# Performance work log

Measured on AMD Instinct MI355X. Metric: run time of the kernel, lower is better.

## Reference

```python
import jax, jax.numpy as jnp
import numpy as np

N, C, H, W = 2, 8, 256, 512
K = 9   # kernel_size
D = 1   # dilation


def setup_inputs() -> dict:
    key = jax.random.key(0)
    k1, k2, k3 = jax.random.split(key, 3)
    x_in = jax.random.normal(k1, (N, C, H, W), dtype=jnp.float32)
    filters = jax.random.normal(k2, (N, K * K, H, W), dtype=jnp.float32)
    filters_biases = jax.random.normal(k3, (N, 1, H, W), dtype=jnp.float32)
    return {"x_in": x_in, "filters": filters, "filters_biases": filters_biases}


def reference(x_in, filters, filters_biases):
    # Dynamic (per-pixel) filtering: out[n,c,h,w] = sum_{i,j} x_pad[n,c,h+i*d,w+j*d] * filters[n,i*K+j,h,w] + bias
    # Equivalent to torch: unfold -> [N,C,K*K,H,W], multiply by filters [N,1,K*K,H,W], sum over K*K, add bias.
    # Fused accumulation over the K*K taps avoids materializing the K*K-times larger im2col tensor.
    k, d = K, D
    p = d * (k - 1) // 2  # 'same' padding used by im2col_layer
    n, c, h, w = x_in.shape
    xp = jnp.pad(x_in, ((0, 0), (0, 0), (p, p), (p, p)))
    out = jnp.zeros_like(x_in)
    for i in range(k):          # fixed small kernel loop (81 taps), unrolled by jit
        for j in range(k):
            tap = filters[:, None, i * k + j]                  # [N,1,H,W]
            out = out + xp[:, :, i * d:i * d + h, j * d:j * d + w] * tap
    return out + filters_biases
```

## Files before the change

### kernel.cpp

```cpp
#include <hip/hip_runtime.h>

#define CC 8
#define HH 256
#define WW 512
#define KK 9
#define XF 272

__global__ __launch_bounds__(256, 4) void dynfilter_kernel(
    const float* __restrict__ x,
    const float* __restrict__ filt,
    const float* __restrict__ fbias,
    float* __restrict__ out)
{
    __shared__ __align__(16) float xs[4][2][2][XF];

    const int tid  = threadIdx.x;
    const int wv   = tid >> 6;
    const int lane = tid & 63;

    const int bid0 = blockIdx.x;
    const int bid  = ((bid0 & 7) << 7) | (bid0 >> 3);

    const int seg = bid & 1;
    const int h   = (bid >> 1) & 255;
    const int n   = bid >> 9;

    const int w0      = seg * 256 + (lane << 2);
    const int wstage0 = seg * 256 - 4;

    const size_t HW = (size_t)HH * WW;
    const int c0 = wv << 1;

    const float* xr0  = x + (size_t)(n * CC + c0)     * HW + wstage0;
    const float* xr1  = x + (size_t)(n * CC + c0 + 1) * HW + wstage0;
    const float* fptr = filt + ((size_t)(n * 81) * HH + h) * WW + w0;

    float acc0[4], acc1[4];
    {
        const float4 b4 = *(const float4*)(fbias + ((size_t)(n * HH + h)) * WW + w0);
        acc0[0]=b4.x; acc0[1]=b4.y; acc0[2]=b4.z; acc0[3]=b4.w;
        acc1[0]=b4.x; acc1[1]=b4.y; acc1[2]=b4.z; acc1[3]=b4.w;
    }

    const int wlo = wstage0 + (lane << 2);
    const int whi = wstage0 + 256 + (lane << 2);
    const bool lo_ok = (unsigned)wlo < (unsigned)WW;
    const bool hi_ok = (lane < 2) && ((unsigned)whi < (unsigned)WW);

    {
        const int hh = h - 4;
        const bool rowok = hh >= 0;
        const float* s0 = xr0 + (size_t)hh * WW;
        const float* s1 = xr1 + (size_t)hh * WW;
        float4 a0 = make_float4(0.f,0.f,0.f,0.f), b0 = a0, a1 = a0, b1 = a0;
        if (rowok && lo_ok) { a0 = *(const float4*)(s0 + (lane<<2));       a1 = *(const float4*)(s1 + (lane<<2)); }
        if (rowok && hi_ok) { b0 = *(const float4*)(s0 + 256 + (lane<<2)); b1 = *(const float4*)(s1 + 256 + (lane<<2)); }
        *(float4*)&xs[wv][0][0][lane<<2] = a0;
        *(float4*)&xs[wv][0][1][lane<<2] = a1;
        if (lane < 2) {
            *(float4*)&xs[wv][0][0][256 + (lane<<2)] = b0;
            *(float4*)&xs[wv][0][1][256 + (lane<<2)] = b1;
        }
    }

    #pragma clang loop unroll(disable)
    for (int i = 0; i < KK; ++i) {
        const int buf = i & 1;

        float4 a0 = make_float4(0.f,0.f,0.f,0.f), b0 = a0, a1 = a0, b1 = a0;
        if (i < KK - 1) {
            const int hh = h - 3 + i;
            const bool rowok = (unsigned)hh < (unsigned)HH;
            const float* s0 = xr0 + (size_t)hh * WW;
            const float* s1 = xr1 + (size_t)hh * WW;
            if (rowok && lo_ok) { a0 = *(const float4*)(s0 + (lane<<2));       a1 = *(const float4*)(s1 + (lane<<2)); }
            if (rowok && hi_ok) { b0 = *(const float4*)(s0 + 256 + (lane<<2)); b1 = *(const float4*)(s1 + 256 + (lane<<2)); }
        }

        float4 f[9];
        {
            const float* fi = fptr + (size_t)i * KK * HW;
            #pragma unroll
            for (int j = 0; j < 9; ++j) f[j] = *(const float4*)(fi + (size_t)j * HW);
        }

        float v0[12], v1[12];
        {
            const float* p0 = &xs[wv][buf][0][lane << 2];
            const float* p1 = &xs[wv][buf][1][lane << 2];
            float4 u;
            u = *(const float4*)(p0 + 0); v0[0]=u.x; v0[1]=u.y; v0[2] =u.z; v0[3] =u.w;
            u = *(const float4*)(p0 + 4); v0[4]=u.x; v0[5]=u.y; v0[6] =u.z; v0[7] =u.w;
            u = *(const float4*)(p0 + 8); v0[8]=u.x; v0[9]=u.y; v0[10]=u.z; v0[11]=u.w;
            u = *(const float4*)(p1 + 0); v1[0]=u.x; v1[1]=u.y; v1[2] =u.z; v1[3] =u.w;
            u = *(const float4*)(p1 + 4); v1[4]=u.x; v1[5]=u.y; v1[6] =u.z; v1[7] =u.w;
            u = *(const float4*)(p1 + 8); v1[8]=u.x; v1[9]=u.y; v1[10]=u.z; v1[11]=u.w;
        }

        #pragma unroll
        for (int j = 0; j < 9; ++j) {
            acc0[0] = fmaf(f[j].x, v0[j+0], acc0[0]);
            acc0[1] = fmaf(f[j].y, v0[j+1], acc0[1]);
            acc0[2] = fmaf(f[j].z, v0[j+2], acc0[2]);
            acc0[3] = fmaf(f[j].w, v0[j+3], acc0[3]);
            acc1[0] = fmaf(f[j].x, v1[j+0], acc1[0]);
            acc1[1] = fmaf(f[j].y, v1[j+1], acc1[1]);
            acc1[2] = fmaf(f[j].z, v1[j+2], acc1[2]);
            acc1[3] = fmaf(f[j].w, v1[j+3], acc1[3]);
        }

        if (i < KK - 1) {
            *(float4*)&xs[wv][buf ^ 1][0][lane<<2] = a0;
            *(float4*)&xs[wv][buf ^ 1][1][lane<<2] = a1;
            if (lane < 2) {
                *(float4*)&xs[wv][buf ^ 1][0][256 + (lane<<2)] = b0;
                *(float4*)&xs[wv][buf ^ 1][1][256 + (lane<<2)] = b1;
            }
        }
    }

    {
        const float4 o0 = make_float4(acc0[0], acc0[1], acc0[2], acc0[3]);
        const float4 o1 = make_float4(acc1[0], acc1[1], acc1[2], acc1[3]);
        *(float4*)(out + ((size_t)(n * CC + c0)     * HH + h) * WW + w0) = o0;
        *(float4*)(out + ((size_t)(n * CC + c0 + 1) * HH + h) * WW + w0) = o1;
    }
}

extern "C" void kernel_launch(void* const* d_in, const int* in_sizes, int n_in,
                              void* d_out, int out_size, void* d_ws, size_t ws_size,
                              hipStream_t stream) {
    const float* x  = (const float*)d_in[0];
    const float* f  = (const float*)d_in[1];
    const float* fb = (const float*)d_in[2];
    float* o = (float*)d_out;
    hipLaunchKernelGGL(dynfilter_kernel, dim3(1024), dim3(256), 0, stream,
                       x, f, fb, o);
}
```

Baseline: 136.6 us.

## Stage filter and input rows into LDS with async global_load_lds pipelining

Filter taps and input rows are now copied straight from global memory into LDS with the gfx950 global_load_lds intrinsic, double-buffered so the next row's loads are in flight while the current row is accumulated. The kernel paces this with explicit vmcnt waits, sched barriers and a block barrier, and the last row is peeled out of the loop. Out-of-range rows and columns are read from clamped addresses and then zeroed in LDS, and the bias is added at the end instead of seeding the accumulator. The aim is to hide global-load latency in a kernel that is limited by memory access. In exchange the code relies on hand-counted wait values that are fragile, adds a per-iteration workgroup barrier, and changes floating-point summation order slightly.

```diff
diff --git a/kernel.cpp b/kernel.cpp
--- a/kernel.cpp
+++ b/kernel.cpp
@@ -4,7 +4,15 @@
 #define HH 256
 #define WW 512
 #define KK 9
+#define HWU (HH * WW)
 #define XF 272
+
+__device__ __forceinline__ void gll16(const float* g, float* l) {
+    __builtin_amdgcn_global_load_lds(
+        (const __attribute__((address_space(1))) float*)g,
+        (__attribute__((address_space(3))) float*)l,
+        16, 0, 0);
+}
 
 __global__ __launch_bounds__(256, 4) void dynfilter_kernel(
     const float* __restrict__ x,
@@ -12,6 +20,7 @@
     const float* __restrict__ fbias,
     float* __restrict__ out)
 {
+    __shared__ __align__(16) float flds[2][KK][256];
     __shared__ __align__(16) float xs[4][2][2][XF];
 
     const int tid  = threadIdx.x;
@@ -28,62 +37,81 @@
     const int w0      = seg * 256 + (lane << 2);
     const int wstage0 = seg * 256 - 4;
 
-    const size_t HW = (size_t)HH * WW;
     const int c0 = wv << 1;
 
-    const float* xr0  = x + (size_t)(n * CC + c0)     * HW + wstage0;
-    const float* xr1  = x + (size_t)(n * CC + c0 + 1) * HW + wstage0;
-    const float* fptr = filt + ((size_t)(n * 81) * HH + h) * WW + w0;
-
-    float acc0[4], acc1[4];
-    {
-        const float4 b4 = *(const float4*)(fbias + ((size_t)(n * HH + h)) * WW + w0);
-        acc0[0]=b4.x; acc0[1]=b4.y; acc0[2]=b4.z; acc0[3]=b4.w;
-        acc1[0]=b4.x; acc1[1]=b4.y; acc1[2]=b4.z; acc1[3]=b4.w;
-    }
-
-    const int wlo = wstage0 + (lane << 2);
-    const int whi = wstage0 + 256 + (lane << 2);
-    const bool lo_ok = (unsigned)wlo < (unsigned)WW;
-    const bool hi_ok = (lane < 2) && ((unsigned)whi < (unsigned)WW);
-
-    {
-        const int hh = h - 4;
-        const bool rowok = hh >= 0;
-        const float* s0 = xr0 + (size_t)hh * WW;
-        const float* s1 = xr1 + (size_t)hh * WW;
-        float4 a0 = make_float4(0.f,0.f,0.f,0.f), b0 = a0, a1 = a0, b1 = a0;
-        if (rowok && lo_ok) { a0 = *(const float4*)(s0 + (lane<<2));       a1 = *(const float4*)(s1 + (lane<<2)); }
-        if (rowok && hi_ok) { b0 = *(const float4*)(s0 + 256 + (lane<<2)); b1 = *(const float4*)(s1 + 256 + (lane<<2)); }
-        *(float4*)&xs[wv][0][0][lane<<2] = a0;
-        *(float4*)&xs[wv][0][1][lane<<2] = a1;
-        if (lane < 2) {
-            *(float4*)&xs[wv][0][0][256 + (lane<<2)] = b0;
-            *(float4*)&xs[wv][0][1][256 + (lane<<2)] = b1;
-        }
-    }
+    const float* fblk = filt + (size_t)(n * 81 * HH + h) * WW + seg * 256;
+    const float* x0   = x + (size_t)(n * CC + c0) * HWU;
+    const float* x1   = x0 + HWU;
+
+    int wA = wstage0 + (lane << 2);
+    int wB = wstage0 + 8 + (lane << 2);
+    wA = wA < 0 ? 0 : (wA > WW - 4 ? WW - 4 : wA);
+    wB = wB < 0 ? 0 : (wB > WW - 4 ? WW - 4 : wB);
+
+    float acc0[4] = {0.f, 0.f, 0.f, 0.f};
+    float acc1[4] = {0.f, 0.f, 0.f, 0.f};
+
+    auto stage_x = [&](int r, int xb) {
+        int hh = h - 4 + r;
+        hh = hh < 0 ? 0 : (hh > HH - 1 ? HH - 1 : hh);
+        const size_t ro = (size_t)hh * WW;
+        float* d0 = &xs[wv][xb][0][0];
+        float* d1 = &xs[wv][xb][1][0];
+        gll16(x0 + ro + wA, d0);
+        gll16(x0 + ro + wB, d0 + 8);
+        gll16(x1 + ro + wA, d1);
+        gll16(x1 + ro + wB, d1 + 8);
+    };
+
+    auto stage_f = [&](const float* frow, int fb) {
+        float* d = &flds[fb][0][0];
+        #pragma unroll
+        for (int j = 0; j < KK; ++j)
+            gll16(frow + (size_t)j * HWU + (lane << 2), d + j * 256);
+    };
+
+    auto fix_x = [&](int xb, int r) {
+        const float4 z = make_float4(0.f, 0.f, 0.f, 0.f);
+        const int hh = h - 4 + r;
+        if ((unsigned)hh >= (unsigned)HH) {
+            *(float4*)&xs[wv][xb][0][lane << 2] = z;
+            *(float4*)&xs[wv][xb][1][lane << 2] = z;
+            if (lane < 2) {
+                *(float4*)&xs[wv][xb][0][256 + (lane << 2)] = z;
+                *(float4*)&xs[wv][xb][1][256 + (lane << 2)] = z;
+            }
+        } else if (lane < 2) {
+            *(float4*)&xs[wv][xb][lane][seg ? 260 : 0] = z;
+        }
+    };
+
+    asm volatile("s_waitcnt vmcnt(0)" ::: "memory");
+
+    stage_f(fblk, 0);
+    stage_x(0, 0);
+    stage_x(1, 1);
+
+    const float* frow = fblk + 9 * HWU;
 
     #pragma clang loop unroll(disable)
-    for (int i = 0; i < KK; ++i) {
+    for (int i = 0; i < KK - 1; ++i) {
         const int buf = i & 1;
 
-        float4 a0 = make_float4(0.f,0.f,0.f,0.f), b0 = a0, a1 = a0, b1 = a0;
-        if (i < KK - 1) {
-            const int hh = h - 3 + i;
-            const bool rowok = (unsigned)hh < (unsigned)HH;
-            const float* s0 = xr0 + (size_t)hh * WW;
-            const float* s1 = xr1 + (size_t)hh * WW;
-            if (rowok && lo_ok) { a0 = *(const float4*)(s0 + (lane<<2));       a1 = *(const float4*)(s1 + (lane<<2)); }
-            if (rowok && hi_ok) { b0 = *(const float4*)(s0 + 256 + (lane<<2)); b1 = *(const float4*)(s1 + 256 + (lane<<2)); }
-        }
+        stage_f(frow, buf ^ 1);
+        frow += 9 * HWU;
+
+        asm volatile("s_waitcnt vmcnt(13)" ::: "memory");
+        __builtin_amdgcn_sched_barrier(0);
+
+        fix_x(buf, i);
+        __builtin_amdgcn_sched_barrier(0);
 
         float4 f[9];
         {
-            const float* fi = fptr + (size_t)i * KK * HW;
+            const float* fp = &flds[buf][0][lane << 2];
             #pragma unroll
-            for (int j = 0; j < 9; ++j) f[j] = *(const float4*)(fi + (size_t)j * HW);
-        }
-
+            for (int j = 0; j < 9; ++j) f[j] = *(const float4*)(fp + j * 256);
+        }
         float v0[12], v1[12];
         {
             const float* p0 = &xs[wv][buf][0][lane << 2];
@@ -109,19 +137,56 @@
             acc1[3] = fmaf(f[j].w, v1[j+3], acc1[3]);
         }
 
-        if (i < KK - 1) {
-            *(float4*)&xs[wv][buf ^ 1][0][lane<<2] = a0;
-            *(float4*)&xs[wv][buf ^ 1][1][lane<<2] = a1;
-            if (lane < 2) {
-                *(float4*)&xs[wv][buf ^ 1][0][256 + (lane<<2)] = b0;
-                *(float4*)&xs[wv][buf ^ 1][1][256 + (lane<<2)] = b1;
-            }
-        }
+        __builtin_amdgcn_sched_barrier(0);
+        stage_x(i + 2, buf);
+
+        __builtin_amdgcn_sched_barrier(0);
+        __builtin_amdgcn_s_barrier();
+        __builtin_amdgcn_sched_barrier(0);
     }
 
+    asm volatile("s_waitcnt vmcnt(4)" ::: "memory");
+    __builtin_amdgcn_sched_barrier(0);
+
+    fix_x(0, 8);
+    __builtin_amdgcn_sched_barrier(0);
+
     {
-        const float4 o0 = make_float4(acc0[0], acc0[1], acc0[2], acc0[3]);
-        const float4 o1 = make_float4(acc1[0], acc1[1], acc1[2], acc1[3]);
+        float4 f[9];
+        const float* fp = &flds[0][0][lane << 2];
+        #pragma unroll
+        for (int j = 0; j < 9; ++j) f[j] = *(const float4*)(fp + j * 256);
+
+        float v0[12], v1[12];
+        const float* p0 = &xs[wv][0][0][lane << 2];
+        const float* p1 = &xs[wv][0][1][lane << 2];
+        float4 u;
+        u = *(const float4*)(p0 + 0); v0[0]=u.x; v0[1]=u.y; v0[2] =u.z; v0[3] =u.w;
+        u = *(const float4*)(p0 + 4); v0[4]=u.x; v0[5]=u.y; v0[6] =u.z; v0[7] =u.w;
+        u = *(const float4*)(p0 + 8); v0[8]=u.x; v0[9]=u.y; v0[10]=u.z; v0[11]=u.w;
+        u = *(const float4*)(p1 + 0); v1[0]=u.x; v1[1]=u.y; v1[2] =u.z; v1[3] =u.w;
+        u = *(const float4*)(p1 + 4); v1[4]=u.x; v1[5]=u.y; v1[6] =u.z; v1[7] =u.w;
+        u = *(const float4*)(p1 + 8); v1[8]=u.x; v1[9]=u.y; v1[10]=u.z; v1[11]=u.w;
+
+        #pragma unroll
+        for (int j = 0; j < 9; ++j) {
+            acc0[0] = fmaf(f[j].x, v0[j+0], acc0[0]);
+            acc0[1] = fmaf(f[j].y, v0[j+1], acc0[1]);
+            acc0[2] = fmaf(f[j].z, v0[j+2], acc0[2]);
+            acc0[3] = fmaf(f[j].w, v0[j+3], acc0[3]);
+            acc1[0] = fmaf(f[j].x, v1[j+0], acc1[0]);
+            acc1[1] = fmaf(f[j].y, v1[j+1], acc1[1]);
+            acc1[2] = fmaf(f[j].z, v1[j+2], acc1[2]);
+            acc1[3] = fmaf(f[j].w, v1[j+3], acc1[3]);
+        }
+    }
+
+    {
+        const float4 b4 = *(const float4*)(fbias + ((size_t)(n * HH + h)) * WW + w0);
+        const float4 o0 = make_float4(acc0[0] + b4.x, acc0[1] + b4.y,
+                                      acc0[2] + b4.z, acc0[3] + b4.w);
+        const float4 o1 = make_float4(acc1[0] + b4.x, acc1[1] + b4.y,
+                                      acc1[2] + b4.z, acc1[3] + b4.w);
         *(float4*)(out + ((size_t)(n * CC + c0)     * HH + h) * WW + w0) = o0;
         *(float4*)(out + ((size_t)(n * CC + c0 + 1) * HH + h) * WW + w0) = o1;
     }
```

Measured after the change: 141.0 us. +3.2%, slower.
